# Kernel optimization log

Measured on AMD Instinct MI355X. Metric: run time of the kernel, lower is better.

The kernel has to match this reference:

```python
import jax, jax.numpy as jnp
import numpy as np

N = 50000
E = 800000
IN_C, HID_C, OUT_C = 5, 64, 32


def setup_inputs() -> dict:
    key = jax.random.key(0)
    ks = jax.random.split(key, 9)
    x = jax.random.normal(ks[0], (N, IN_C), dtype=jnp.float32)
    edge_index = jax.random.randint(ks[1], (2, E), 0, N, dtype=jnp.int64)
    # SAGEConv params: lin_l (neighbor path, has bias), lin_r (root path, no bias)
    def lin(k, fan_out, fan_in):
        s = 1.0 / np.sqrt(fan_in)
        return jax.random.uniform(k, (fan_out, fan_in), jnp.float32, -s, s)
    W1l = lin(ks[2], HID_C, IN_C); b1 = jnp.zeros((HID_C,), jnp.float32); W1r = lin(ks[3], HID_C, IN_C)
    W2l = lin(ks[4], HID_C, HID_C); b2 = jnp.zeros((HID_C,), jnp.float32); W2r = lin(ks[5], HID_C, HID_C)
    W3l = lin(ks[6], OUT_C, HID_C); b3 = jnp.zeros((OUT_C,), jnp.float32); W3r = lin(ks[7], OUT_C, HID_C)
    return {"x": x, "edge_index": edge_index,
            "W1l": W1l, "b1": b1, "W1r": W1r,
            "W2l": W2l, "b2": b2, "W2r": W2r,
            "W3l": W3l, "b3": b3, "W3r": W3r}


def _sage_conv(x, src, dst, inv_deg, Wl, bl, Wr):
    # PyG SAGEConv (aggr='mean'): out = lin_l(mean_j x_j) + lin_r(x)
    msg = x[src]                                          # [E, d_in] gather
    agg = jax.ops.segment_sum(msg, dst, num_segments=N)   # [N, d_in] scatter-add
    mean = agg * inv_deg                                  # mean aggregation
    return mean @ Wl.T + bl + x @ Wr.T


def reference(x, edge_index, W1l, b1, W1r, W2l, b2, W2r, W3l, b3, W3r):
    src, dst = edge_index[0], edge_index[1]
    deg = jax.ops.segment_sum(jnp.ones((E,), x.dtype), dst, num_segments=N)
    inv_deg = (1.0 / jnp.maximum(deg, 1.0))[:, None]      # [N, 1]
    h = jax.nn.relu(_sage_conv(x, src, dst, inv_deg, W1l, b1, W1r))
    # F.dropout(p=0.2, training=self.training): identity in eval mode
    h = jax.nn.relu(_sage_conv(h, src, dst, inv_deg, W2l, b2, W2r))
    out = _sage_conv(h, src, dst, inv_deg, W3l, b3, W3r)
    return out
```

## Files before the change

### kernel.cpp

```cpp
#include <hip/hip_runtime.h>
#include <hip/hip_fp16.h>


#define N_NODES 50000
#define N_EDGES 800000
#define IN_C 5
#define HID_C 64
#define OUT_C 32

#define NB 196
#define BCAP 6144
#define BWG 800
#define BCH (N_EDGES / BWG)

typedef __attribute__((ext_vector_type(8))) short bf16x8;
typedef __attribute__((ext_vector_type(4))) float f32x4;

__device__ __forceinline__ int rfl(int v) { return __builtin_amdgcn_readfirstlane(v); }
__device__ __forceinline__ float lanebc(float v, int l) {
    return __int_as_float(__builtin_amdgcn_readlane(__float_as_int(v), l));
}
__device__ __forceinline__ unsigned short f2bf(float f) {
    unsigned u = __float_as_uint(f);
    return (unsigned short)((u + 0x7fffu + ((u >> 16) & 1u)) >> 16);
}
__device__ __forceinline__ float bf2f(unsigned short b) {
    return __uint_as_float(((unsigned)b) << 16);
}
__device__ __forceinline__ float2 unpk_h2(unsigned u) {
    __half2 h = *(__half2*)&u;
    return __half22float2(h);
}


__global__ __launch_bounds__(256) void k_prep(
    const float* __restrict__ W2l, const float* __restrict__ W2r,
    const float* __restrict__ W3l, const float* __restrict__ W3r,
    unsigned short* __restrict__ W2hi, unsigned short* __restrict__ W2lo,
    unsigned short* __restrict__ W3hi, unsigned short* __restrict__ W3lo,
    int* __restrict__ gcur) {
    if (blockIdx.x == 0 && threadIdx.x < NB) gcur[threadIdx.x] = 0;
    const int t = blockIdx.x * 256 + threadIdx.x;
    const int stride = gridDim.x * 256;
    for (int p = t; p < 64 * 128; p += stride) {
        int j = p >> 7, k = p & 127;
        float w = (k < 64) ? W2l[j * 64 + k] : W2r[j * 64 + (k - 64)];
        unsigned short h = f2bf(w);
        W2hi[p] = h;
        W2lo[p] = f2bf(w - bf2f(h));
    }
    for (int p = t; p < 32 * 128; p += stride) {
        int j = p >> 7, k = p & 127;
        float w = (k < 64) ? W3l[j * 64 + k] : W3r[j * 64 + (k - 64)];
        unsigned short h = f2bf(w);
        W3hi[p] = h;
        W3lo[p] = f2bf(w - bf2f(h));
    }
}


__global__ __launch_bounds__(256) void k_bucket(const int* __restrict__ ei,
                                                int* __restrict__ gcur,
                                                unsigned* __restrict__ ebuf) {
    __shared__ int hist[NB];
    __shared__ int loff[NB];
    __shared__ int cur[NB];
    __shared__ int gbase[NB];
    __shared__ int scanb[256];
    __shared__ unsigned ev0[BCH];
    __shared__ unsigned stage[BCH];
    const int t = threadIdx.x;
    const int c0 = blockIdx.x * BCH;

    if (t < NB) hist[t] = 0;
    __syncthreads();
    for (int i = t; i < BCH; i += 256) {
        int s = ei[c0 + i];
        int d = ei[N_EDGES + c0 + i];
        ev0[i] = ((unsigned)d << 16) | (unsigned)s;
        atomicAdd(&hist[d >> 8], 1);
    }
    __syncthreads();
    scanb[t] = (t < NB) ? hist[t] : 0;
    __syncthreads();
#pragma unroll
    for (int o = 1; o < 256; o <<= 1) {
        int v = scanb[t];
        int a = (t >= o) ? scanb[t - o] : 0;
        __syncthreads();
        scanb[t] = v + a;
        __syncthreads();
    }
    if (t < NB) {
        int ex = (t == 0) ? 0 : scanb[t - 1];
        loff[t] = ex;
        cur[t] = ex;
        gbase[t] = atomicAdd(&gcur[t], hist[t]);
    }
    __syncthreads();
    for (int i = t; i < BCH; i += 256) {
        unsigned ev = ev0[i];
        int b = ev >> 24;
        int p = atomicAdd(&cur[b], 1);
        stage[p] = ev;
    }
    __syncthreads();
    for (int i = t; i < BCH; i += 256) {
        unsigned ev = stage[i];
        int b = ev >> 24;
        int pos = gbase[b] + (i - loff[b]);
        if (pos < BCAP) ebuf[b * BCAP + pos] = ev;
    }
}

__global__ __launch_bounds__(256) void k_bsort(const int* __restrict__ gcur,
                                               const unsigned* __restrict__ ebuf,
                                               int* __restrict__ row_off,
                                               float* __restrict__ inv_deg,
                                               int* __restrict__ srcs) {
    __shared__ int sc[256];
    __shared__ int cnt[256];
    __shared__ int loff[256];
    __shared__ int cur[256];
    __shared__ int stage[BCAP];
    const int t = threadIdx.x;
    const int b = blockIdx.x;

    sc[t] = (t < NB) ? gcur[t] : 0;
    __syncthreads();
#pragma unroll
    for (int o = 1; o < 256; o <<= 1) {
        int v = sc[t];
        int a = (t >= o) ? sc[t - o] : 0;
        __syncthreads();
        sc[t] = v + a;
        __syncthreads();
    }
    const int base = (b == 0) ? 0 : sc[b - 1];
    const int nraw = gcur[b];
    const int n = nraw < BCAP ? nraw : BCAP;
    const int node0 = b << 8;
    const unsigned* eb = ebuf + b * BCAP;

    cnt[t] = 0;
    __syncthreads();
    for (int i = t; i < n; i += 256) atomicAdd(&cnt[(eb[i] >> 16) & 255], 1);
    __syncthreads();
    loff[t] = cnt[t];
    __syncthreads();
#pragma unroll
    for (int o = 1; o < 256; o <<= 1) {
        int v = loff[t];
        int a = (t >= o) ? loff[t - o] : 0;
        __syncthreads();
        loff[t] = v + a;
        __syncthreads();
    }
    int ex = loff[t] - cnt[t];
    cur[t] = ex;
    int node = node0 + t;
    if (node < N_NODES) {
        row_off[node] = base + ex;
        int d = cnt[t];
        inv_deg[node] = 1.0f / (float)(d > 1 ? d : 1);
    }
    if (b == 0 && t == 0) row_off[N_NODES] = N_EDGES;
    __syncthreads();
    for (int i = t; i < n; i += 256) {
        unsigned ev = eb[i];
        int p = atomicAdd(&cur[(ev >> 16) & 255], 1);
        stage[p] = (int)(ev & 0xFFFFu);
    }
    __syncthreads();
    for (int i = t; i < n; i += 256) srcs[base + i] = stage[i];
}


__global__ __launch_bounds__(256) void k_layer1(
    const float* __restrict__ x, const int* __restrict__ row_off,
    const int* __restrict__ srcs, const float* __restrict__ inv_deg,
    const float* __restrict__ W1l, const float* __restrict__ b1,
    const float* __restrict__ W1r, __half* __restrict__ h1) {
    const int t = threadIdx.x;
    const int lane = t & 63;
    const int v = blockIdx.x * 4 + (t >> 6);
    if (v >= N_NODES) return;
    const int sub = lane >> 3;
    const int c = lane & 7;

    float wl[IN_C], wr[IN_C];
#pragma unroll
    for (int i = 0; i < IN_C; ++i) {
        wl[i] = W1l[lane * IN_C + i];
        wr[i] = W1r[lane * IN_C + i];
    }
    float bb = b1[lane];

    int beg = rfl(row_off[v]);
    int end = rfl(row_off[v + 1]);
    float xv = (lane < IN_C) ? x[v * IN_C + lane] : 0.f;
    float idg = inv_deg[v];
    float sum = 0.f;
    for (int e = beg; e < end; e += 8) {
        int o = e + sub;
        if (o < end && c < IN_C) sum += x[srcs[o] * IN_C + c];
    }
    sum += __shfl_xor(sum, 8, 64);
    sum += __shfl_xor(sum, 16, 64);
    sum += __shfl_xor(sum, 32, 64);
    float summ = sum * idg;
    float acc = bb;
#pragma unroll
    for (int i = 0; i < IN_C; ++i) {
        acc += wl[i] * lanebc(summ, i);
        acc += wr[i] * lanebc(xv, i);
    }
    h1[v * HID_C + lane] = __float2half(fmaxf(acc, 0.f));
}


template <typename T> __device__ __forceinline__ T cvt_out(float v);
template <> __device__ __forceinline__ float cvt_out<float>(float v) { return v; }
template <> __device__ __forceinline__ __half cvt_out<__half>(float v) { return __float2half(v); }

template <int DOUT, bool RELU, typename OutT>
__global__ __launch_bounds__(256) void k_fused(
    const __half* __restrict__ h, const int* __restrict__ row_off,
    const int* __restrict__ srcs, const float* __restrict__ inv_deg,
    const unsigned short* __restrict__ Whi, const unsigned short* __restrict__ Wlo,
    const float* __restrict__ bias, OutT* __restrict__ out) {
    constexpr int AP = 152;
    __shared__ __align__(16) unsigned short Ah[32][AP];
    __shared__ __align__(16) unsigned short Al[32][AP];
    const int t = threadIdx.x;
    const int lane = t & 63;
    const int w = t >> 6;
    const int ns = lane >> 3;
    const int cg = lane & 7;
    const int node0 = blockIdx.x * 32;
    const int m = w * 8 + ns;
    const int v = node0 + m;
    const bool valid = v < N_NODES;
    const uint4* h4 = (const uint4*)h;

    int beg = 0, deg = 0;
    float idg = 0.f;
    uint4 ur = make_uint4(0u, 0u, 0u, 0u);
    if (valid) {
        beg = row_off[v];
        deg = row_off[v + 1] - beg;
        idg = inv_deg[v];
        ur = h4[v * 8 + cg];
    }

    const int* sp = srcs + beg;
    const int last = (deg > 0) ? (deg - 1) : 0;
#define SIDX(K) sp[(K) < last ? (K) : last]
    int j0 = SIDX(0), j1 = SIDX(1), j2 = SIDX(2), j3 = SIDX(3);
    int j4 = SIDX(4), j5 = SIDX(5), j6 = SIDX(6), j7 = SIDX(7);

    float s0 = 0.f, s1 = 0.f, s2 = 0.f, s3 = 0.f;
    float s4 = 0.f, s5 = 0.f, s6 = 0.f, s7 = 0.f;
    for (int k = 0; k < deg; k += 8) {
        uint4 u0 = h4[j0 * 8 + cg];
        uint4 u1 = h4[j1 * 8 + cg];
        uint4 u2 = h4[j2 * 8 + cg];
        uint4 u3 = h4[j3 * 8 + cg];
        uint4 u4 = h4[j4 * 8 + cg];
        uint4 u5 = h4[j5 * 8 + cg];
        uint4 u6 = h4[j6 * 8 + cg];
        uint4 u7 = h4[j7 * 8 + cg];
        float w1 = (k + 1 < deg) ? 1.f : 0.f;
        float w2 = (k + 2 < deg) ? 1.f : 0.f;
        float w3 = (k + 3 < deg) ? 1.f : 0.f;
        float w4 = (k + 4 < deg) ? 1.f : 0.f;
        float w5 = (k + 5 < deg) ? 1.f : 0.f;
        float w6 = (k + 6 < deg) ? 1.f : 0.f;
        float w7 = (k + 7 < deg) ? 1.f : 0.f;
        j0 = SIDX(k + 8);  j1 = SIDX(k + 9);  j2 = SIDX(k + 10); j3 = SIDX(k + 11);
        j4 = SIDX(k + 12); j5 = SIDX(k + 13); j6 = SIDX(k + 14); j7 = SIDX(k + 15);
        {
            float2 a = unpk_h2(u0.x), b = unpk_h2(u0.y);
            float2 c = unpk_h2(u0.z), d = unpk_h2(u0.w);
            s0 += a.x; s1 += a.y; s2 += b.x; s3 += b.y;
            s4 += c.x; s5 += c.y; s6 += d.x; s7 += d.y;
        }
#define ACCW(U, W)                                                     \
        {                                                              \
            float2 a = unpk_h2(U.x), b = unpk_h2(U.y);                 \
            float2 c = unpk_h2(U.z), d = unpk_h2(U.w);                 \
            s0 = fmaf(a.x, W, s0); s1 = fmaf(a.y, W, s1);              \
            s2 = fmaf(b.x, W, s2); s3 = fmaf(b.y, W, s3);              \
            s4 = fmaf(c.x, W, s4); s5 = fmaf(c.y, W, s5);              \
            s6 = fmaf(d.x, W, s6); s7 = fmaf(d.y, W, s7);              \
        }
        ACCW(u1, w1) ACCW(u2, w2) ACCW(u3, w3)
        ACCW(u4, w4) ACCW(u5, w5) ACCW(u6, w6) ACCW(u7, w7)
#undef ACCW
    }
#undef SIDX

    float m0 = s0 * idg, m1 = s1 * idg, m2 = s2 * idg, m3 = s3 * idg;
    float m4 = s4 * idg, m5 = s5 * idg, m6 = s6 * idg, m7 = s7 * idg;

    {
        unsigned short a0 = f2bf(m0), a1 = f2bf(m1), a2 = f2bf(m2), a3 = f2bf(m3);
        unsigned short a4 = f2bf(m4), a5 = f2bf(m5), a6 = f2bf(m6), a7 = f2bf(m7);
        uint4 hi, lo;
        hi.x = (unsigned)a0 | ((unsigned)a1 << 16);
        hi.y = (unsigned)a2 | ((unsigned)a3 << 16);
        hi.z = (unsigned)a4 | ((unsigned)a5 << 16);
        hi.w = (unsigned)a6 | ((unsigned)a7 << 16);
        lo.x = (unsigned)f2bf(m0 - bf2f(a0)) | ((unsigned)f2bf(m1 - bf2f(a1)) << 16);
        lo.y = (unsigned)f2bf(m2 - bf2f(a2)) | ((unsigned)f2bf(m3 - bf2f(a3)) << 16);
        lo.z = (unsigned)f2bf(m4 - bf2f(a4)) | ((unsigned)f2bf(m5 - bf2f(a5)) << 16);
        lo.w = (unsigned)f2bf(m6 - bf2f(a6)) | ((unsigned)f2bf(m7 - bf2f(a7)) << 16);
        *(uint4*)&Ah[m][cg * 8] = hi;
        *(uint4*)&Al[m][cg * 8] = lo;
    }
    {
        float2 p0 = unpk_h2(ur.x), p1 = unpk_h2(ur.y);
        float2 p2 = unpk_h2(ur.z), p3 = unpk_h2(ur.w);
        unsigned short a0 = f2bf(p0.x), a1 = f2bf(p0.y), a2 = f2bf(p1.x), a3 = f2bf(p1.y);
        unsigned short a4 = f2bf(p2.x), a5 = f2bf(p2.y), a6 = f2bf(p3.x), a7 = f2bf(p3.y);
        uint4 hi, lo;
        hi.x = (unsigned)a0 | ((unsigned)a1 << 16);
        hi.y = (unsigned)a2 | ((unsigned)a3 << 16);
        hi.z = (unsigned)a4 | ((unsigned)a5 << 16);
        hi.w = (unsigned)a6 | ((unsigned)a7 << 16);
        lo.x = (unsigned)f2bf(p0.x - bf2f(a0)) | ((unsigned)f2bf(p0.y - bf2f(a1)) << 16);
        lo.y = (unsigned)f2bf(p1.x - bf2f(a2)) | ((unsigned)f2bf(p1.y - bf2f(a3)) << 16);
        lo.z = (unsigned)f2bf(p2.x - bf2f(a4)) | ((unsigned)f2bf(p2.y - bf2f(a5)) << 16);
        lo.w = (unsigned)f2bf(p3.x - bf2f(a6)) | ((unsigned)f2bf(p3.y - bf2f(a7)) << 16);
        *(uint4*)&Ah[m][64 + cg * 8] = hi;
        *(uint4*)&Al[m][64 + cg * 8] = lo;
    }
    __syncthreads();

    constexpr int CT = DOUT / 16;
    constexpr int NTILES = 2 * CT;
    const int r = lane & 15;
    const int quad = lane >> 4;
#pragma unroll
    for (int ti = w; ti < NTILES; ti += 4) {
        const int n = ti % CT;
        const int rh = ti / CT;
        f32x4 acc = (f32x4){0.f, 0.f, 0.f, 0.f};
#pragma unroll
        for (int ks = 0; ks < 4; ++ks) {
            bf16x8 ah = *(const bf16x8*)&Ah[rh * 16 + r][ks * 32 + quad * 8];
            bf16x8 al = *(const bf16x8*)&Al[rh * 16 + r][ks * 32 + quad * 8];
            const size_t wb = ((size_t)(n * 16 + r)) * 128 + ks * 32 + quad * 8;
            bf16x8 bh = *(const bf16x8*)(Whi + wb);
            bf16x8 bl = *(const bf16x8*)(Wlo + wb);
            acc = __builtin_amdgcn_mfma_f32_16x16x32_bf16(ah, bh, acc, 0, 0, 0);
            acc = __builtin_amdgcn_mfma_f32_16x16x32_bf16(ah, bl, acc, 0, 0, 0);
            acc = __builtin_amdgcn_mfma_f32_16x16x32_bf16(al, bh, acc, 0, 0, 0);
        }
        float bv = bias[n * 16 + r];
#pragma unroll
        for (int g = 0; g < 4; ++g) {
            int node = node0 + rh * 16 + quad * 4 + g;
            if (node < N_NODES) {
                float vv = acc[g] + bv;
                if (RELU) vv = fmaxf(vv, 0.f);
                out[(size_t)node * DOUT + n * 16 + r] = cvt_out<OutT>(vv);
            }
        }
    }
}


extern "C" void kernel_launch(void* const* d_in, const int* in_sizes, int n_in,
                              void* d_out, int out_size, void* d_ws, size_t ws_size,
                              hipStream_t stream) {
    const float* x   = (const float*)d_in[0];
    const int*   ei  = (const int*)d_in[1];
    const float* W1l = (const float*)d_in[2];
    const float* b1  = (const float*)d_in[3];
    const float* W1r = (const float*)d_in[4];
    const float* W2l = (const float*)d_in[5];
    const float* b2  = (const float*)d_in[6];
    const float* W2r = (const float*)d_in[7];
    const float* W3l = (const float*)d_in[8];
    const float* b3  = (const float*)d_in[9];
    const float* W3r = (const float*)d_in[10];

    char* ws = (char*)d_ws;
    size_t off = 0;
    auto alloc = [&](size_t bytes) -> char* {
        char* p = ws + off;
        off += (bytes + 255) & ~(size_t)255;
        return p;
    };
    int*      gcur   = (int*)alloc(NB * sizeof(int));
    int*      rowoff = (int*)alloc((N_NODES + 1) * sizeof(int));
    float*    invdeg = (float*)alloc(N_NODES * sizeof(float));
    int*      srcs   = (int*)alloc(N_EDGES * sizeof(int));
    unsigned* ebuf   = (unsigned*)alloc((size_t)NB * BCAP * sizeof(unsigned));
    __half*   h1     = (__half*)alloc((size_t)N_NODES * HID_C * sizeof(__half));
    __half*   h2     = (__half*)alloc((size_t)N_NODES * HID_C * sizeof(__half));
    unsigned short* W2hi = (unsigned short*)alloc(64 * 128 * 2);
    unsigned short* W2lo = (unsigned short*)alloc(64 * 128 * 2);
    unsigned short* W3hi = (unsigned short*)alloc(32 * 128 * 2);
    unsigned short* W3lo = (unsigned short*)alloc(32 * 128 * 2);

    k_prep<<<dim3(48), dim3(256), 0, stream>>>(W2l, W2r, W3l, W3r,
                                               W2hi, W2lo, W3hi, W3lo, gcur);
    k_bucket<<<dim3(BWG), dim3(256), 0, stream>>>(ei, gcur, ebuf);
    k_bsort<<<dim3(NB), dim3(256), 0, stream>>>(gcur, ebuf, rowoff, invdeg, srcs);

    k_layer1<<<dim3(N_NODES / 4), dim3(256), 0, stream>>>(
        x, rowoff, srcs, invdeg, W1l, b1, W1r, h1);

    const int FT = (N_NODES + 31) / 32;
    k_fused<HID_C, true, __half><<<dim3(FT), dim3(256), 0, stream>>>(
        h1, rowoff, srcs, invdeg, W2hi, W2lo, b2, h2);

    k_fused<OUT_C, false, float><<<dim3(FT), dim3(256), 0, stream>>>(
        h2, rowoff, srcs, invdeg, W3hi, W3lo, b3, (float*)d_out);
}
```

Baseline: 176.5 us.

## Reorder layer 3 as transform-then-aggregate, fused into layer 2

Layer 3 now applies the linear maps before aggregating. The layer-2 kernel immediately multiplies its h2 tile by a stacked [W3l; W3r] matrix. It writes a 32-wide fp16 neighbor projection and an fp32 root projection plus bias, instead of writing the 64-wide h2. A new aggregation kernel then gathers only 32 fp16 channels per edge and adds the root term. This halves the gather width of the last layer and drops the h2 round trip. In exchange it rounds the projected neighbor features to fp16 and adds an extra shared-memory pass and syncs in the fused kernel.

```diff
diff --git a/kernel.cpp b/kernel.cpp
--- a/kernel.cpp
+++ b/kernel.cpp
@@ -37,7 +37,7 @@
     const float* __restrict__ W2l, const float* __restrict__ W2r,
     const float* __restrict__ W3l, const float* __restrict__ W3r,
     unsigned short* __restrict__ W2hi, unsigned short* __restrict__ W2lo,
-    unsigned short* __restrict__ W3hi, unsigned short* __restrict__ W3lo,
+    unsigned short* __restrict__ W3zhi, unsigned short* __restrict__ W3zlo,
     int* __restrict__ gcur) {
     if (blockIdx.x == 0 && threadIdx.x < NB) gcur[threadIdx.x] = 0;
     const int t = blockIdx.x * 256 + threadIdx.x;
@@ -49,12 +49,12 @@
         W2hi[p] = h;
         W2lo[p] = f2bf(w - bf2f(h));
     }
-    for (int p = t; p < 32 * 128; p += stride) {
-        int j = p >> 7, k = p & 127;
-        float w = (k < 64) ? W3l[j * 64 + k] : W3r[j * 64 + (k - 64)];
+    for (int p = t; p < 64 * 64; p += stride) {
+        int j = p >> 6, k = p & 63;
+        float w = (j < 32) ? W3l[j * 64 + k] : W3r[(j - 32) * 64 + k];
         unsigned short h = f2bf(w);
-        W3hi[p] = h;
-        W3lo[p] = f2bf(w - bf2f(h));
+        W3zhi[p] = h;
+        W3zlo[p] = f2bf(w - bf2f(h));
     }
 }
 
@@ -219,16 +219,14 @@
 }
 
 
-template <typename T> __device__ __forceinline__ T cvt_out(float v);
-template <> __device__ __forceinline__ float cvt_out<float>(float v) { return v; }
-template <> __device__ __forceinline__ __half cvt_out<__half>(float v) { return __float2half(v); }
-
-template <int DOUT, bool RELU, typename OutT>
-__global__ __launch_bounds__(256) void k_fused(
+__global__ __launch_bounds__(256) void k_fused2(
     const __half* __restrict__ h, const int* __restrict__ row_off,
     const int* __restrict__ srcs, const float* __restrict__ inv_deg,
-    const unsigned short* __restrict__ Whi, const unsigned short* __restrict__ Wlo,
-    const float* __restrict__ bias, OutT* __restrict__ out) {
+    const unsigned short* __restrict__ W2hi, const unsigned short* __restrict__ W2lo,
+    const float* __restrict__ b2,
+    const unsigned short* __restrict__ W3zhi, const unsigned short* __restrict__ W3zlo,
+    const float* __restrict__ b3,
+    __half* __restrict__ z3l, float* __restrict__ z3r) {
     constexpr int AP = 152;
     __shared__ __align__(16) unsigned short Ah[32][AP];
     __shared__ __align__(16) unsigned short Al[32][AP];
@@ -337,36 +335,136 @@
     }
     __syncthreads();
 
-    constexpr int CT = DOUT / 16;
-    constexpr int NTILES = 2 * CT;
     const int r = lane & 15;
     const int quad = lane >> 4;
-#pragma unroll
-    for (int ti = w; ti < NTILES; ti += 4) {
-        const int n = ti % CT;
-        const int rh = ti / CT;
-        f32x4 acc = (f32x4){0.f, 0.f, 0.f, 0.f};
-#pragma unroll
-        for (int ks = 0; ks < 4; ++ks) {
-            bf16x8 ah = *(const bf16x8*)&Ah[rh * 16 + r][ks * 32 + quad * 8];
-            bf16x8 al = *(const bf16x8*)&Al[rh * 16 + r][ks * 32 + quad * 8];
-            const size_t wb = ((size_t)(n * 16 + r)) * 128 + ks * 32 + quad * 8;
-            bf16x8 bh = *(const bf16x8*)(Whi + wb);
-            bf16x8 bl = *(const bf16x8*)(Wlo + wb);
-            acc = __builtin_amdgcn_mfma_f32_16x16x32_bf16(ah, bh, acc, 0, 0, 0);
-            acc = __builtin_amdgcn_mfma_f32_16x16x32_bf16(ah, bl, acc, 0, 0, 0);
-            acc = __builtin_amdgcn_mfma_f32_16x16x32_bf16(al, bh, acc, 0, 0, 0);
+    f32x4 accA = (f32x4){0.f, 0.f, 0.f, 0.f};
+    f32x4 accB = (f32x4){0.f, 0.f, 0.f, 0.f};
+#pragma unroll
+    for (int ks = 0; ks < 4; ++ks) {
+        bf16x8 ah0 = *(const bf16x8*)&Ah[r][ks * 32 + quad * 8];
+        bf16x8 al0 = *(const bf16x8*)&Al[r][ks * 32 + quad * 8];
+        bf16x8 ah1 = *(const bf16x8*)&Ah[16 + r][ks * 32 + quad * 8];
+        bf16x8 al1 = *(const bf16x8*)&Al[16 + r][ks * 32 + quad * 8];
+        const size_t wb = ((size_t)(w * 16 + r)) * 128 + ks * 32 + quad * 8;
+        bf16x8 bh = *(const bf16x8*)(W2hi + wb);
+        bf16x8 bl = *(const bf16x8*)(W2lo + wb);
+        accA = __builtin_amdgcn_mfma_f32_16x16x32_bf16(ah0, bh, accA, 0, 0, 0);
+        accA = __builtin_amdgcn_mfma_f32_16x16x32_bf16(ah0, bl, accA, 0, 0, 0);
+        accA = __builtin_amdgcn_mfma_f32_16x16x32_bf16(al0, bh, accA, 0, 0, 0);
+        accB = __builtin_amdgcn_mfma_f32_16x16x32_bf16(ah1, bh, accB, 0, 0, 0);
+        accB = __builtin_amdgcn_mfma_f32_16x16x32_bf16(ah1, bl, accB, 0, 0, 0);
+        accB = __builtin_amdgcn_mfma_f32_16x16x32_bf16(al1, bh, accB, 0, 0, 0);
+    }
+    const float bv2 = b2[w * 16 + r];
+    float h2A[4], h2B[4];
+#pragma unroll
+    for (int g = 0; g < 4; ++g) {
+        h2A[g] = fmaxf(accA[g] + bv2, 0.f);
+        h2B[g] = fmaxf(accB[g] + bv2, 0.f);
+    }
+    __syncthreads();
+
+#pragma unroll
+    for (int g = 0; g < 4; ++g) {
+        unsigned short hiA = f2bf(h2A[g]);
+        Ah[quad * 4 + g][w * 16 + r] = hiA;
+        Al[quad * 4 + g][w * 16 + r] = f2bf(h2A[g] - bf2f(hiA));
+        unsigned short hiB = f2bf(h2B[g]);
+        Ah[16 + quad * 4 + g][w * 16 + r] = hiB;
+        Al[16 + quad * 4 + g][w * 16 + r] = f2bf(h2B[g] - bf2f(hiB));
+    }
+    __syncthreads();
+
+    f32x4 zA = (f32x4){0.f, 0.f, 0.f, 0.f};
+    f32x4 zB = (f32x4){0.f, 0.f, 0.f, 0.f};
+#pragma unroll
+    for (int ks = 0; ks < 2; ++ks) {
+        bf16x8 ah0 = *(const bf16x8*)&Ah[r][ks * 32 + quad * 8];
+        bf16x8 al0 = *(const bf16x8*)&Al[r][ks * 32 + quad * 8];
+        bf16x8 ah1 = *(const bf16x8*)&Ah[16 + r][ks * 32 + quad * 8];
+        bf16x8 al1 = *(const bf16x8*)&Al[16 + r][ks * 32 + quad * 8];
+        const size_t wb = ((size_t)(w * 16 + r)) * 64 + ks * 32 + quad * 8;
+        bf16x8 bh = *(const bf16x8*)(W3zhi + wb);
+        bf16x8 bl = *(const bf16x8*)(W3zlo + wb);
+        zA = __builtin_amdgcn_mfma_f32_16x16x32_bf16(ah0, bh, zA, 0, 0, 0);
+        zA = __builtin_amdgcn_mfma_f32_16x16x32_bf16(ah0, bl, zA, 0, 0, 0);
+        zA = __builtin_amdgcn_mfma_f32_16x16x32_bf16(al0, bh, zA, 0, 0, 0);
+        zB = __builtin_amdgcn_mfma_f32_16x16x32_bf16(ah1, bh, zB, 0, 0, 0);
+        zB = __builtin_amdgcn_mfma_f32_16x16x32_bf16(ah1, bl, zB, 0, 0, 0);
+        zB = __builtin_amdgcn_mfma_f32_16x16x32_bf16(al1, bh, zB, 0, 0, 0);
+    }
+    const int j = w * 16 + r;
+    const float badd = (j >= 32) ? b3[j - 32] : 0.f;
+#pragma unroll
+    for (int g = 0; g < 4; ++g) {
+        int nodeA = node0 + quad * 4 + g;
+        int nodeB = node0 + 16 + quad * 4 + g;
+        float vA = zA[g] + badd;
+        float vB = zB[g] + badd;
+        if (nodeA < N_NODES) {
+            if (j < 32) z3l[(size_t)nodeA * 32 + j] = __float2half(vA);
+            else        z3r[(size_t)nodeA * 32 + (j - 32)] = vA;
         }
-        float bv = bias[n * 16 + r];
-#pragma unroll
-        for (int g = 0; g < 4; ++g) {
-            int node = node0 + rh * 16 + quad * 4 + g;
-            if (node < N_NODES) {
-                float vv = acc[g] + bv;
-                if (RELU) vv = fmaxf(vv, 0.f);
-                out[(size_t)node * DOUT + n * 16 + r] = cvt_out<OutT>(vv);
-            }
+        if (nodeB < N_NODES) {
+            if (j < 32) z3l[(size_t)nodeB * 32 + j] = __float2half(vB);
+            else        z3r[(size_t)nodeB * 32 + (j - 32)] = vB;
         }
+    }
+}
+
+
+__global__ __launch_bounds__(256) void k_agg3(
+    const int* __restrict__ row_off, const int* __restrict__ srcs,
+    const float* __restrict__ inv_deg,
+    const __half* __restrict__ z3l, const float* __restrict__ z3r,
+    float* __restrict__ out) {
+    const int t = threadIdx.x;
+    const int lane = t & 63;
+    const int v = blockIdx.x * 4 + (t >> 6);
+    if (v >= N_NODES) return;
+    const int slot = lane >> 2;
+    const int cg = lane & 3;
+
+    const int beg = rfl(row_off[v]);
+    const int end = rfl(row_off[v + 1]);
+    const int deg = end - beg;
+    const float idg = inv_deg[v];
+    const uint4* z4 = (const uint4*)z3l;
+
+    float s0 = 0.f, s1 = 0.f, s2 = 0.f, s3 = 0.f;
+    float s4 = 0.f, s5 = 0.f, s6 = 0.f, s7 = 0.f;
+    for (int k = 0; k < deg; k += 16) {
+        int o = beg + k + slot;
+        int oc = (o < end) ? o : (end - 1);
+        int jn = srcs[oc];
+        uint4 u = z4[jn * 4 + cg];
+        float wk = (k + slot < deg) ? 1.f : 0.f;
+        float2 a = unpk_h2(u.x), b = unpk_h2(u.y);
+        float2 c = unpk_h2(u.z), d = unpk_h2(u.w);
+        s0 = fmaf(a.x, wk, s0); s1 = fmaf(a.y, wk, s1);
+        s2 = fmaf(b.x, wk, s2); s3 = fmaf(b.y, wk, s3);
+        s4 = fmaf(c.x, wk, s4); s5 = fmaf(c.y, wk, s5);
+        s6 = fmaf(d.x, wk, s6); s7 = fmaf(d.y, wk, s7);
+    }
+#pragma unroll
+    for (int off = 4; off <= 32; off <<= 1) {
+        s0 += __shfl_xor(s0, off, 64); s1 += __shfl_xor(s1, off, 64);
+        s2 += __shfl_xor(s2, off, 64); s3 += __shfl_xor(s3, off, 64);
+        s4 += __shfl_xor(s4, off, 64); s5 += __shfl_xor(s5, off, 64);
+        s6 += __shfl_xor(s6, off, 64); s7 += __shfl_xor(s7, off, 64);
+    }
+    if (lane < 4) {
+        const float4* zr4 = (const float4*)(z3r + (size_t)v * 32);
+        float4 r0 = zr4[lane * 2];
+        float4 r1 = zr4[lane * 2 + 1];
+        float4 o0, o1;
+        o0.x = fmaf(s0, idg, r0.x); o0.y = fmaf(s1, idg, r0.y);
+        o0.z = fmaf(s2, idg, r0.z); o0.w = fmaf(s3, idg, r0.w);
+        o1.x = fmaf(s4, idg, r1.x); o1.y = fmaf(s5, idg, r1.y);
+        o1.z = fmaf(s6, idg, r1.z); o1.w = fmaf(s7, idg, r1.w);
+        float4* op = (float4*)(out + (size_t)v * 32);
+        op[lane * 2] = o0;
+        op[lane * 2 + 1] = o1;
     }
 }
 
@@ -399,14 +497,15 @@
     int*      srcs   = (int*)alloc(N_EDGES * sizeof(int));
     unsigned* ebuf   = (unsigned*)alloc((size_t)NB * BCAP * sizeof(unsigned));
     __half*   h1     = (__half*)alloc((size_t)N_NODES * HID_C * sizeof(__half));
-    __half*   h2     = (__half*)alloc((size_t)N_NODES * HID_C * sizeof(__half));
-    unsigned short* W2hi = (unsigned short*)alloc(64 * 128 * 2);
-    unsigned short* W2lo = (unsigned short*)alloc(64 * 128 * 2);
-    unsigned short* W3hi = (unsigned short*)alloc(32 * 128 * 2);
-    unsigned short* W3lo = (unsigned short*)alloc(32 * 128 * 2);
+    __half*   z3l    = (__half*)alloc((size_t)N_NODES * OUT_C * sizeof(__half));
+    float*    z3r    = (float*)alloc((size_t)N_NODES * OUT_C * sizeof(float));
+    unsigned short* W2hi  = (unsigned short*)alloc(64 * 128 * 2);
+    unsigned short* W2lo  = (unsigned short*)alloc(64 * 128 * 2);
+    unsigned short* W3zhi = (unsigned short*)alloc(64 * 64 * 2);
+    unsigned short* W3zlo = (unsigned short*)alloc(64 * 64 * 2);
 
     k_prep<<<dim3(48), dim3(256), 0, stream>>>(W2l, W2r, W3l, W3r,
-                                               W2hi, W2lo, W3hi, W3lo, gcur);
+                                               W2hi, W2lo, W3zhi, W3zlo, gcur);
     k_bucket<<<dim3(BWG), dim3(256), 0, stream>>>(ei, gcur, ebuf);
     k_bsort<<<dim3(NB), dim3(256), 0, stream>>>(gcur, ebuf, rowoff, invdeg, srcs);
 
@@ -414,9 +513,9 @@
         x, rowoff, srcs, invdeg, W1l, b1, W1r, h1);
 
     const int FT = (N_NODES + 31) / 32;
-    k_fused<HID_C, true, __half><<<dim3(FT), dim3(256), 0, stream>>>(
-        h1, rowoff, srcs, invdeg, W2hi, W2lo, b2, h2);
-
-    k_fused<OUT_C, false, float><<<dim3(FT), dim3(256), 0, stream>>>(
-        h2, rowoff, srcs, invdeg, W3hi, W3lo, b3, (float*)d_out);
-}
+    k_fused2<<<dim3(FT), dim3(256), 0, stream>>>(
+        h1, rowoff, srcs, invdeg, W2hi, W2lo, b2, W3zhi, W3zlo, b3, z3l, z3r);
+
+    k_agg3<<<dim3((N_NODES + 3) / 4), dim3(256), 0, stream>>>(
+        rowoff, srcs, invdeg, z3l, z3r, (float*)d_out);
+}
```

Measured after the change: 178.4 us. About the same (+1.1%).
